# Performance work log

Measured on AMD Instinct MI355X. Metric: run time of the kernel, lower is better.

## Reference

```python
import jax, jax.numpy as jnp
import numpy as np


def setup_inputs() -> dict:
    key = jax.random.key(0)
    k1, k2 = jax.random.split(key)
    # [batch, seq, in_features] activations
    x = jax.random.normal(k1, (4, 4096, 2048), dtype=jnp.float32)
    # fp32 master weight [out_features, in_features]; quantized inside reference
    weight = jax.random.normal(k2, (2048, 2048), dtype=jnp.float32) * 0.02
    return {"x": x, "weight": weight}


def reference(x, weight):
    num_bits = 8
    Qn = -(2 ** (num_bits - 1))       # -128
    Qp = 2 ** (num_bits - 1) - 1      # 127

    # Per-row absmax int8 activation quantization (activation_quant)
    si = Qp / jnp.clip(jnp.max(jnp.abs(x), axis=-1, keepdims=True), 1e-5)  # [B,S,1]
    qx = jnp.clip(jnp.round(x * si), Qn, Qp)  # int8 values held in fp32 (exact)

    # Ternary weight quantization (weight_quant): sw scalar = 1/mean|W|
    sw = 1.0 / jnp.clip(jnp.mean(jnp.abs(weight)), 1e-5)
    qw = jnp.clip(jnp.round(weight * sw), -1.0, 1.0)  # {-1,0,1}

    acc = jnp.einsum("bsk,nk->bsn", qx, qw)  # [B,S,out]

    # post_quant_process: dequantize by si and sw, cast to half
    out = ((acc / si) / sw).astype(jnp.float16)
    return out
```

## Files before the change

kernel.cpp:

```cpp
#include <hip/hip_runtime.h>

#define K_DIM 2048
#define N_DIM 2048
#define M_DIM 16384

typedef int v4i __attribute__((ext_vector_type(4)));
typedef int v16i __attribute__((ext_vector_type(16)));


__device__ __forceinline__ void lds16(const void* g, void* l) {
    __builtin_amdgcn_global_load_lds(
        (const __attribute__((address_space(1))) unsigned int*)g,
        (__attribute__((address_space(3))) unsigned int*)l,
        16, 0, 0);
}

__global__ __launch_bounds__(256) void k_wsum(const float* __restrict__ w,
                                              double* __restrict__ part) {
    int tid = blockIdx.x * 256 + threadIdx.x;
    const float4* w4 = (const float4*)w;
    double s = 0.0;
    for (int i = tid; i < (N_DIM * K_DIM / 4); i += 262144) {
        float4 v = w4[i];
        s += (double)fabsf(v.x);
        s += (double)fabsf(v.y);
        s += (double)fabsf(v.z);
        s += (double)fabsf(v.w);
    }
#pragma unroll
    for (int off = 32; off; off >>= 1) s += __shfl_xor(s, off, 64);
    __shared__ double sp[4];
    int lane = threadIdx.x & 63, wv = threadIdx.x >> 6;
    if (lane == 0) sp[wv] = s;
    __syncthreads();
    if (threadIdx.x == 0) part[blockIdx.x] = sp[0] + sp[1] + sp[2] + sp[3];
}

__global__ __launch_bounds__(256) void k_quant_w(const float* __restrict__ w,
                                                 signed char* __restrict__ qw_t,
                                                 const double* __restrict__ part,
                                                 float* __restrict__ invsw_out) {
    double s = part[threadIdx.x] + part[threadIdx.x + 256] +
               part[threadIdx.x + 512] + part[threadIdx.x + 768];
#pragma unroll
    for (int off = 32; off; off >>= 1) s += __shfl_xor(s, off, 64);
    __shared__ double sp[4];
    __shared__ float s_invsw;
    __shared__ int lbuf[2048];
    int lane = threadIdx.x & 63, wv = threadIdx.x >> 6;
    if (lane == 0) sp[wv] = s;
    __syncthreads();
    if (threadIdx.x == 0) {
        double total = sp[0] + sp[1] + sp[2] + sp[3];
        float mean = (float)(total * (1.0 / (double)(N_DIM * K_DIM)));
        s_invsw = fmaxf(mean, 1e-5f);
        if (blockIdx.x == 0) *invsw_out = s_invsw;
    }
    __syncthreads();
    float sw = 1.0f / s_invsw;

    int row = blockIdx.x * 4 + wv;
    const float4* wr_ = (const float4*)(w + (size_t)row * K_DIM);
    int k16 = (lane >> 2) & 3, b = lane & 3, ksBase = lane >> 4;
#pragma unroll
    for (int c = 0; c < 8; c++) {
        float4 v = wr_[c * 64 + lane];
        int q0 = (int)fminf(fmaxf(rintf(v.x * sw), -1.f), 1.f);
        int q1 = (int)fminf(fmaxf(rintf(v.y * sw), -1.f), 1.f);
        int q2 = (int)fminf(fmaxf(rintf(v.z * sw), -1.f), 1.f);
        int q3 = (int)fminf(fmaxf(rintf(v.w * sw), -1.f), 1.f);
        int q = (q0 & 255) | ((q1 & 255) << 8) | ((q2 & 255) << 16) | ((q3 & 255) << 24);
        int ks = 4 * c + ksBase;
        lbuf[(ks * 4 + k16) * 16 + wv * 4 + b] = q;
    }
    __syncthreads();
    int bn = (blockIdx.x * 4) >> 7, ri0 = (blockIdx.x * 4) & 127;
    int* qdst = (int*)(qw_t + (size_t)bn * 262144 + (size_t)ri0 * 16);
#pragma unroll
    for (int r = 0; r < 8; r++) {
        int chunk = r * 16 + (threadIdx.x >> 4);
        int i16 = threadIdx.x & 15;
        int ks = chunk >> 2, kk = chunk & 3;
        int row4 = i16 >> 2, bb = i16 & 3;
        qdst[ks * 2048 + kk * 512 + row4 * 4 + bb] = lbuf[chunk * 16 + i16];
    }
}

__global__ __launch_bounds__(256) void k_quant_x(const float* __restrict__ x,
                                                 signed char* __restrict__ qx_t,
                                                 float* __restrict__ si_out) {
    __shared__ int lbuf[2048];
    int wv = threadIdx.x >> 6, lane = threadIdx.x & 63;
    int row = blockIdx.x * 4 + wv;
    const float4* xr = (const float4*)(x + (size_t)row * K_DIM);
    float4 v[8];
    float mx = 0.f;
#pragma unroll
    for (int c = 0; c < 8; c++) {
        v[c] = xr[c * 64 + lane];
        mx = fmaxf(mx, fmaxf(fmaxf(fabsf(v[c].x), fabsf(v[c].y)),
                             fmaxf(fabsf(v[c].z), fabsf(v[c].w))));
    }
#pragma unroll
    for (int off = 32; off; off >>= 1) mx = fmaxf(mx, __shfl_xor(mx, off, 64));
    float si = 127.0f / fmaxf(mx, 1e-5f);
    if (lane == 0) si_out[row] = si;

    int k16 = (lane >> 2) & 3, b = lane & 3, ksBase = lane >> 4;
#pragma unroll
    for (int c = 0; c < 8; c++) {
        int q0 = (int)fminf(fmaxf(rintf(v[c].x * si), -128.f), 127.f);
        int q1 = (int)fminf(fmaxf(rintf(v[c].y * si), -128.f), 127.f);
        int q2 = (int)fminf(fmaxf(rintf(v[c].z * si), -128.f), 127.f);
        int q3 = (int)fminf(fmaxf(rintf(v[c].w * si), -128.f), 127.f);
        int q = (q0 & 255) | ((q1 & 255) << 8) | ((q2 & 255) << 16) | ((q3 & 255) << 24);
        int ks = 4 * c + ksBase;
        lbuf[(ks * 4 + k16) * 16 + wv * 4 + b] = q;
    }
    __syncthreads();
    int bm = (blockIdx.x * 4) >> 8, ri0 = (blockIdx.x * 4) & 255;
    int* qdst = (int*)(qx_t + (size_t)bm * 524288 + (size_t)ri0 * 16);
#pragma unroll
    for (int r = 0; r < 8; r++) {
        int chunk = r * 16 + (threadIdx.x >> 4);
        int i16 = threadIdx.x & 15;
        int ks = chunk >> 2, kk = chunk & 3;
        int row4 = i16 >> 2, bb = i16 & 3;
        qdst[ks * 4096 + kk * 1024 + row4 * 4 + bb] = lbuf[chunk * 16 + i16];
    }
}

__global__ __launch_bounds__(256, 2) void k_gemm(const signed char* __restrict__ qx_t,
                                                 const signed char* __restrict__ qw_t,
                                                 const float* __restrict__ si,
                                                 const float* __restrict__ invsw_p,
                                                 float* __restrict__ out) {
    __shared__ __align__(16) signed char As[3][16384];
    __shared__ __align__(16) signed char Bs[2][8192];
    const int t = threadIdx.x;
    const int lane = t & 63, wv = t >> 6;
    const int wr = wv >> 1, wc = wv & 1;
    const int l31 = lane & 31, lh = lane >> 5;

    const int wg = blockIdx.x;
    const int swz = (wg & 7) * 128 + (wg >> 3);
    const int bn = swz & 15, bm = swz >> 4;

    const signed char* aT = qx_t + (size_t)bm * 524288;
    const signed char* bT = qw_t + (size_t)bn * 262144;
    const int t16 = t << 4;

#define STAGE_A(buf, ksv)                                    \
    {                                                        \
        const signed char* aS = aT + ((size_t)(ksv) << 14);  \
        signed char* Ad = As[buf];                           \
        lds16(aS + t16,         Ad + t16);                   \
        lds16(aS + 4096 + t16,  Ad + 4096 + t16);            \
        lds16(aS + 8192 + t16,  Ad + 8192 + t16);            \
        lds16(aS + 12288 + t16, Ad + 12288 + t16);           \
    }
#define STAGE_B(buf, ksv)                                    \
    {                                                        \
        const signed char* bS = bT + ((size_t)(ksv) << 13);  \
        signed char* Bd = Bs[buf];                           \
        lds16(bS + t16,         Bd + t16);                   \
        lds16(bS + 4096 + t16,  Bd + 4096 + t16);            \
    }

    v16i acc[4][2] = {};

#define READ_HALF(AC, BC, h, af, bf)                                                                 \
    _Pragma("unroll") for (int mt = 0; mt < 4; mt++)                                                 \
        af[mt] = *(const v4i*)(As[AC] + ((((h) * 2 + lh) * 256 + wr * 128 + mt * 32 + l31) << 4));   \
    _Pragma("unroll") for (int nt = 0; nt < 2; nt++)                                                 \
        bf[nt] = *(const v4i*)(Bs[BC] + ((((h) * 2 + lh) * 128 + wc * 64 + nt * 32 + l31) << 4));

#define MFMA8(af, bf)                                                                                \
    __builtin_amdgcn_s_setprio(1);                                                                   \
    _Pragma("unroll") for (int mt = 0; mt < 4; mt++)                                                 \
        _Pragma("unroll") for (int nt = 0; nt < 2; nt++)                                             \
            acc[mt][nt] = __builtin_amdgcn_mfma_i32_32x32x32_i8(af[mt], bf[nt], acc[mt][nt], 0, 0, 0); \
    __builtin_amdgcn_s_setprio(0);

#define ITER(ksv, AC, BC, AS, BS)                            \
    {                                                        \
        asm volatile("s_waitcnt vmcnt(4)" ::: "memory");     \
        __builtin_amdgcn_s_barrier();                        \
        __builtin_amdgcn_sched_barrier(0);                   \
        v4i af[4], bf[2];                                    \
        READ_HALF(AC, BC, 0, af, bf);                        \
        STAGE_B(BS, (ksv) + 1);                              \
        MFMA8(af, bf);                                       \
        READ_HALF(AC, BC, 1, af, bf);                        \
        STAGE_A(AS, (ksv) + 2);                              \
        MFMA8(af, bf);                                       \
    }

    STAGE_B(0, 0);
    STAGE_A(0, 0);
    STAGE_A(1, 1);

    for (int ks = 0; ks < 30; ks += 6) {
        ITER(ks + 0, 0, 0, 2, 1);
        ITER(ks + 1, 1, 1, 0, 0);
        ITER(ks + 2, 2, 0, 1, 1);
        ITER(ks + 3, 0, 1, 2, 0);
        ITER(ks + 4, 1, 0, 0, 1);
        ITER(ks + 5, 2, 1, 1, 0);
    }

    {
        asm volatile("s_waitcnt vmcnt(4)" ::: "memory");
        __builtin_amdgcn_s_barrier();
        __builtin_amdgcn_sched_barrier(0);
        v4i af[4], bf[2];
        READ_HALF(0, 0, 0, af, bf);
        STAGE_B(1, 31);
        MFMA8(af, bf);
        READ_HALF(0, 0, 1, af, bf);
        MFMA8(af, bf);
    }
    {
        asm volatile("s_waitcnt vmcnt(0)" ::: "memory");
        __builtin_amdgcn_s_barrier();
        __builtin_amdgcn_sched_barrier(0);
        v4i af[4], bf[2];
        READ_HALF(1, 1, 0, af, bf);
        MFMA8(af, bf);
        READ_HALF(1, 1, 1, af, bf);
        MFMA8(af, bf);
    }

#undef ITER
#undef MFMA8
#undef READ_HALF
#undef STAGE_A
#undef STAGE_B

    float invsw = *invsw_p;
#pragma unroll
    for (int mt = 0; mt < 4; mt++) {
        int rowb = bm * 256 + wr * 128 + mt * 32 + (lh << 2);
        float sc[16];
#pragma unroll
        for (int r = 0; r < 16; r++)
            sc[r] = invsw / si[rowb + (r & 3) + ((r >> 2) << 3)];
#pragma unroll
        for (int nt = 0; nt < 2; nt++) {
            int col = bn * 128 + wc * 64 + nt * 32 + l31;
#pragma unroll
            for (int r = 0; r < 16; r++) {
                int row = rowb + (r & 3) + ((r >> 2) << 3);
                float vv = (float)acc[mt][nt][r] * sc[r];
                out[(size_t)row * N_DIM + col] = (float)(_Float16)vv;
            }
        }
    }
}

extern "C" void kernel_launch(void* const* d_in, const int* in_sizes, int n_in,
                              void* d_out, int out_size, void* d_ws, size_t ws_size,
                              hipStream_t stream) {
    const float* x = (const float*)d_in[0];
    const float* w = (const float*)d_in[1];
    float* out = (float*)d_out;
    char* ws = (char*)d_ws;

    double* part = (double*)ws;
    float* invsw = (float*)(ws + 8192);
    float* si = (float*)(ws + 12288);
    signed char* qw_t = (signed char*)(ws + 12288 + 65536);
    signed char* qx_t = qw_t + (size_t)N_DIM * K_DIM;

    k_wsum<<<1024, 256, 0, stream>>>(w, part);
    k_quant_x<<<4096, 256, 0, stream>>>(x, qx_t, si);
    k_quant_w<<<512, 256, 0, stream>>>(w, qw_t, part, invsw);
    k_gemm<<<1024, 256, 0, stream>>>(qx_t, qw_t, si, invsw, out);
}
```

Baseline: 312.7 us.

## Load A fragments directly into registers, drop A LDS staging

A tile fragments are now read straight from global memory into registers and double-buffered in VGPRs, so only the B tile goes through LDS. Each wave owns 64 rows across all 128 columns (a 2x4 MFMA layout instead of 4x2). This removes the 48KB A buffers and the LDS traffic for A, which lowers shared memory use and could raise occupancy. In exchange every k-step waits on vmcnt(0), leaving only one stage of prefetch, and the direct global loads add latency exposure and register pressure.

```diff
diff --git a/kernel.cpp b/kernel.cpp
--- a/kernel.cpp
+++ b/kernel.cpp
@@ -135,11 +135,9 @@
                                                  const float* __restrict__ si,
                                                  const float* __restrict__ invsw_p,
                                                  float* __restrict__ out) {
-    __shared__ __align__(16) signed char As[3][16384];
     __shared__ __align__(16) signed char Bs[2][8192];
     const int t = threadIdx.x;
     const int lane = t & 63, wv = t >> 6;
-    const int wr = wv >> 1, wc = wv & 1;
     const int l31 = lane & 31, lh = lane >> 5;
 
     const int wg = blockIdx.x;
@@ -149,105 +147,73 @@
     const signed char* aT = qx_t + (size_t)bm * 524288;
     const signed char* bT = qw_t + (size_t)bn * 262144;
     const int t16 = t << 4;
-
-#define STAGE_A(buf, ksv)                                    \
-    {                                                        \
-        const signed char* aS = aT + ((size_t)(ksv) << 14);  \
-        signed char* Ad = As[buf];                           \
-        lds16(aS + t16,         Ad + t16);                   \
-        lds16(aS + 4096 + t16,  Ad + 4096 + t16);            \
-        lds16(aS + 8192 + t16,  Ad + 8192 + t16);            \
-        lds16(aS + 12288 + t16, Ad + 12288 + t16);           \
-    }
+    const signed char* aP = aT + ((size_t)lh << 12) + (((wv << 6) + l31) << 4);
+    const int bL = (lh << 11) + (l31 << 4);
+
 #define STAGE_B(buf, ksv)                                    \
     {                                                        \
         const signed char* bS = bT + ((size_t)(ksv) << 13);  \
         signed char* Bd = Bs[buf];                           \
-        lds16(bS + t16,         Bd + t16);                   \
-        lds16(bS + 4096 + t16,  Bd + 4096 + t16);            \
-    }
-
-    v16i acc[4][2] = {};
-
-#define READ_HALF(AC, BC, h, af, bf)                                                                 \
-    _Pragma("unroll") for (int mt = 0; mt < 4; mt++)                                                 \
-        af[mt] = *(const v4i*)(As[AC] + ((((h) * 2 + lh) * 256 + wr * 128 + mt * 32 + l31) << 4));   \
-    _Pragma("unroll") for (int nt = 0; nt < 2; nt++)                                                 \
-        bf[nt] = *(const v4i*)(Bs[BC] + ((((h) * 2 + lh) * 128 + wc * 64 + nt * 32 + l31) << 4));
-
-#define MFMA8(af, bf)                                                                                \
-    __builtin_amdgcn_s_setprio(1);                                                                   \
-    _Pragma("unroll") for (int mt = 0; mt < 4; mt++)                                                 \
-        _Pragma("unroll") for (int nt = 0; nt < 2; nt++)                                             \
-            acc[mt][nt] = __builtin_amdgcn_mfma_i32_32x32x32_i8(af[mt], bf[nt], acc[mt][nt], 0, 0, 0); \
-    __builtin_amdgcn_s_setprio(0);
-
-#define ITER(ksv, AC, BC, AS, BS)                            \
-    {                                                        \
-        asm volatile("s_waitcnt vmcnt(4)" ::: "memory");     \
-        __builtin_amdgcn_s_barrier();                        \
-        __builtin_amdgcn_sched_barrier(0);                   \
-        v4i af[4], bf[2];                                    \
-        READ_HALF(AC, BC, 0, af, bf);                        \
-        STAGE_B(BS, (ksv) + 1);                              \
-        MFMA8(af, bf);                                       \
-        READ_HALF(AC, BC, 1, af, bf);                        \
-        STAGE_A(AS, (ksv) + 2);                              \
-        MFMA8(af, bf);                                       \
-    }
-
+        lds16(bS + t16,        Bd + t16);                    \
+        lds16(bS + 4096 + t16, Bd + 4096 + t16);             \
+    }
+
+#define LOAD_A(af, ksv)                                                          \
+    _Pragma("unroll") for (int h = 0; h < 2; h++)                                \
+        _Pragma("unroll") for (int mt = 0; mt < 2; mt++)                         \
+            af[h][mt] = *(const v4i*)(aP + ((size_t)(ksv) << 14) + (h << 13) + (mt << 9));
+
+    v16i acc[2][4] = {};
+
+#define ITER(ksv, afC, afN, bufC)                                                                     \
+    {                                                                                                 \
+        asm volatile("s_waitcnt vmcnt(0)" ::: "memory");                                              \
+        __builtin_amdgcn_s_barrier();                                                                 \
+        __builtin_amdgcn_sched_barrier(0);                                                            \
+        if ((ksv) < 31) {                                                                             \
+            LOAD_A(afN, (ksv) + 1);                                                                   \
+            STAGE_B((bufC) ^ 1, (ksv) + 1);                                                           \
+        }                                                                                             \
+        _Pragma("unroll")                                                                             \
+        for (int h = 0; h < 2; h++) {                                                                 \
+            v4i bf[4];                                                                                \
+            _Pragma("unroll")                                                                         \
+            for (int nt = 0; nt < 4; nt++)                                                            \
+                bf[nt] = *(const v4i*)(Bs[bufC] + bL + (h << 12) + (nt << 9));                        \
+            __builtin_amdgcn_s_setprio(1);                                                            \
+            _Pragma("unroll")                                                                         \
+            for (int mt = 0; mt < 2; mt++)                                                            \
+                _Pragma("unroll")                                                                     \
+                for (int nt = 0; nt < 4; nt++)                                                        \
+                    acc[mt][nt] = __builtin_amdgcn_mfma_i32_32x32x32_i8(afC[h][mt], bf[nt], acc[mt][nt], 0, 0, 0); \
+            __builtin_amdgcn_s_setprio(0);                                                            \
+        }                                                                                             \
+    }
+
+    v4i afA[2][2], afB[2][2];
+    LOAD_A(afA, 0);
     STAGE_B(0, 0);
-    STAGE_A(0, 0);
-    STAGE_A(1, 1);
-
-    for (int ks = 0; ks < 30; ks += 6) {
-        ITER(ks + 0, 0, 0, 2, 1);
-        ITER(ks + 1, 1, 1, 0, 0);
-        ITER(ks + 2, 2, 0, 1, 1);
-        ITER(ks + 3, 0, 1, 2, 0);
-        ITER(ks + 4, 1, 0, 0, 1);
-        ITER(ks + 5, 2, 1, 1, 0);
-    }
-
-    {
-        asm volatile("s_waitcnt vmcnt(4)" ::: "memory");
-        __builtin_amdgcn_s_barrier();
-        __builtin_amdgcn_sched_barrier(0);
-        v4i af[4], bf[2];
-        READ_HALF(0, 0, 0, af, bf);
-        STAGE_B(1, 31);
-        MFMA8(af, bf);
-        READ_HALF(0, 0, 1, af, bf);
-        MFMA8(af, bf);
-    }
-    {
-        asm volatile("s_waitcnt vmcnt(0)" ::: "memory");
-        __builtin_amdgcn_s_barrier();
-        __builtin_amdgcn_sched_barrier(0);
-        v4i af[4], bf[2];
-        READ_HALF(1, 1, 0, af, bf);
-        MFMA8(af, bf);
-        READ_HALF(1, 1, 1, af, bf);
-        MFMA8(af, bf);
+
+    for (int ks = 0; ks < 32; ks += 2) {
+        ITER(ks,     afA, afB, 0);
+        ITER(ks + 1, afB, afA, 1);
     }
 
 #undef ITER
-#undef MFMA8
-#undef READ_HALF
-#undef STAGE_A
+#undef LOAD_A
 #undef STAGE_B
 
     float invsw = *invsw_p;
 #pragma unroll
-    for (int mt = 0; mt < 4; mt++) {
-        int rowb = bm * 256 + wr * 128 + mt * 32 + (lh << 2);
+    for (int mt = 0; mt < 2; mt++) {
+        int rowb = bm * 256 + wv * 64 + mt * 32 + (lh << 2);
         float sc[16];
 #pragma unroll
         for (int r = 0; r < 16; r++)
             sc[r] = invsw / si[rowb + (r & 3) + ((r >> 2) << 3)];
 #pragma unroll
-        for (int nt = 0; nt < 2; nt++) {
-            int col = bn * 128 + wc * 64 + nt * 32 + l31;
+        for (int nt = 0; nt < 4; nt++) {
+            int col = bn * 128 + nt * 32 + l31;
 #pragma unroll
             for (int r = 0; r < 16; r++) {
                 int row = rowb + (r & 3) + ((r >> 2) << 3);
```

Result: no change. 313.5 us (+0.3%).
